# Kernel optimization log

Measured on AMD Instinct MI355X. Metric: run time of the kernel, lower is better.

Reference implementation:

```python
import jax, jax.numpy as jnp
import numpy as np

N_NODES = 100000
N_EDGES = 20000
N_PAIRS = 640000
IN_CH = 128
HEADS = 4
OUT_CH = 32


def setup_inputs() -> dict:
    key = jax.random.key(0)
    k1, k2, k3, k4, k5 = jax.random.split(key, 5)
    X = jax.random.normal(k1, (N_NODES, IN_CH), dtype=jnp.float32)
    # nn.Linear(in, H*C, bias=False); stored as [in, H*C] so X0 = X @ W
    W = jax.random.normal(k2, (IN_CH, HEADS * OUT_CH), dtype=jnp.float32) * (1.0 / np.sqrt(IN_CH))
    stdv = (6.0 / (HEADS + OUT_CH)) ** 0.5
    att_e = jax.random.uniform(k3, (1, HEADS, OUT_CH), dtype=jnp.float32, minval=-stdv, maxval=stdv)
    vertex = jax.random.randint(k4, (N_PAIRS,), 0, N_NODES, dtype=jnp.int64)
    edges = jax.random.randint(k5, (N_PAIRS,), 0, N_EDGES, dtype=jnp.int64)
    return {"X": X, "W": W, "att_e": att_e, "vertex": vertex, "edges": edges}


def reference(X, W, att_e, vertex, edges):
    N = X.shape[0]
    H, C = HEADS, OUT_CH
    X0 = X @ W                                  # [N, H*C]
    Xv_hc = X0.reshape(N, H, C)
    Xve = Xv_hc[vertex]                          # [M, H, C] gather
    # scatter-mean over hyperedges
    esum = jax.ops.segment_sum(Xve, edges, num_segments=N_EDGES)
    ecnt = jax.ops.segment_sum(jnp.ones((Xve.shape[0],), X.dtype), edges, num_segments=N_EDGES)
    Xe = esum / jnp.maximum(ecnt, 1.0)[:, None, None]   # [E, H, C]
    alpha_e = (Xe * att_e).sum(-1)               # [E, H]
    a_ev = alpha_e[edges]                        # [M, H]
    alpha = jax.nn.leaky_relu(a_ev, 0.01)
    # per-vertex softmax over incident hyperedges
    amax = jax.ops.segment_max(alpha, vertex, num_segments=N)
    alpha = jnp.exp(alpha - amax[vertex])
    asum = jax.ops.segment_sum(alpha, vertex, num_segments=N)
    alpha = alpha / (asum[vertex] + 1e-8)
    Xev = Xe[edges] * alpha[:, :, None]          # [M, H, C]
    Xv = jax.ops.segment_sum(Xev, vertex, num_segments=N)
    return Xv.reshape(N, H * C) + X0
```

## Files before the change

### kernel.cpp

```cpp
#include <hip/hip_runtime.h>
#include <hip/hip_bf16.h>

#define N_NODES 100000
#define N_EDGES 20000
#define N_PAIRS 640000
#define CH 128
#define HEADS 4
#define MAXDV 32

#define NG_GEMM 1563
#define NCHUNK 125
#define ECHUNK 5120
#define EW 5120
#define VWR 5000
#define NRANGE 5
#define VBIN_R 20000

#define OFF_X0H   0UL
#define OFF_XEH   25600000UL
#define OFF_LRE   30720000UL
#define OFF_LRV5  31360000UL
#define OFF_BLKE  34560000UL
#define OFF_BLKV  37120000UL
#define OFF_WT    50222400UL
#define OFF_ALPHA 50255168UL
#define OFF_OFFE  50575168UL
#define OFF_ENDE  50657088UL
#define OFF_OFFV  50739008UL
#define OFF_ENDV  51139008UL
#define OFF_PIDXE 51539008UL
#define OFF_PIDXV 54099008UL
#define OFF_TOT   56659008UL

typedef __attribute__((ext_vector_type(8))) short bf16x8;
typedef __attribute__((ext_vector_type(4))) float f32x4;

__device__ inline short f2bf(float f) {
    __hip_bfloat16 h = __float2bfloat16(f);
    return reinterpret_cast<short&>(h);
}
__device__ inline float bflo(unsigned w) { return __uint_as_float(w << 16); }
__device__ inline float bfhi(unsigned w) { return __uint_as_float(w & 0xffff0000u); }

__global__ __launch_bounds__(256) void k_wprep(const float* __restrict__ W,
                                               short* __restrict__ Wt,
                                               int* __restrict__ totals) {
    if (blockIdx.x == 0 && threadIdx.x < 2) totals[threadIdx.x] = 0;
    const int idx = blockIdx.x * 256 + threadIdx.x;
    const int n = idx >> 7, k = idx & 127;
    Wt[n * CH + k] = f2bf(W[k * CH + n]);
}

__device__ inline void gemm_body(int gb, const float* __restrict__ X,
                                 const short* __restrict__ Wt,
                                 short* __restrict__ X0h) {
    const int t = threadIdx.x;
    const int wave = t >> 6, lane = t & 63;
    const int r0 = gb * 64 + (wave >> 1) * 32;
    const int c0 = (wave & 1) * 64;
    const int lrow = lane & 15, lk8 = (lane >> 4) * 8;
    const int row0 = min(r0 + lrow, N_NODES - 1);
    const int row1 = min(r0 + 16 + lrow, N_NODES - 1);
    const float* px0 = &X[(size_t)row0 * CH + lk8];
    const float* px1 = &X[(size_t)row1 * CH + lk8];
    const short* pw0 = &Wt[(size_t)(c0 + lrow) * CH + lk8];

    f32x4 acc[2][4] = {};

    float4 xa[2][2]; bf16x8 bb[4];
    xa[0][0] = *(const float4*)(px0); xa[0][1] = *(const float4*)(px0 + 4);
    xa[1][0] = *(const float4*)(px1); xa[1][1] = *(const float4*)(px1 + 4);
#pragma unroll
    for (int n = 0; n < 4; ++n) bb[n] = *(const bf16x8*)(pw0 + n * 16 * CH);

#pragma unroll
    for (int kk = 0; kk < 4; ++kk) {
        float4 xn[2][2]; bf16x8 bn[4];
        if (kk < 3) {
            const int ks = (kk + 1) * 32;
            xn[0][0] = *(const float4*)(px0 + ks); xn[0][1] = *(const float4*)(px0 + ks + 4);
            xn[1][0] = *(const float4*)(px1 + ks); xn[1][1] = *(const float4*)(px1 + ks + 4);
#pragma unroll
            for (int n = 0; n < 4; ++n) bn[n] = *(const bf16x8*)(pw0 + n * 16 * CH + ks);
        }
        bf16x8 a[2];
#pragma unroll
        for (int m = 0; m < 2; ++m) {
            a[m][0] = f2bf(xa[m][0].x); a[m][1] = f2bf(xa[m][0].y);
            a[m][2] = f2bf(xa[m][0].z); a[m][3] = f2bf(xa[m][0].w);
            a[m][4] = f2bf(xa[m][1].x); a[m][5] = f2bf(xa[m][1].y);
            a[m][6] = f2bf(xa[m][1].z); a[m][7] = f2bf(xa[m][1].w);
        }
#pragma unroll
        for (int m = 0; m < 2; ++m)
#pragma unroll
            for (int n = 0; n < 4; ++n)
                acc[m][n] = __builtin_amdgcn_mfma_f32_16x16x32_bf16(a[m], bb[n], acc[m][n], 0, 0, 0);
        if (kk < 3) {
#pragma unroll
            for (int m = 0; m < 2; ++m) { xa[m][0] = xn[m][0]; xa[m][1] = xn[m][1]; }
#pragma unroll
            for (int n = 0; n < 4; ++n) bb[n] = bn[n];
        }
    }

#pragma unroll
    for (int m = 0; m < 2; ++m) {
#pragma unroll
        for (int reg = 0; reg < 4; ++reg) {
            const int row = r0 + m * 16 + (lane >> 4) * 4 + reg;
            if (row < N_NODES) {
#pragma unroll
                for (int n = 0; n < 4; ++n)
                    X0h[(size_t)row * CH + c0 + n * 16 + (lane & 15)] = f2bf(acc[m][n][reg]);
            }
        }
    }
}

__global__ __launch_bounds__(256) void k_phase1(const float* __restrict__ X,
                                                const short* __restrict__ Wt,
                                                short* __restrict__ X0h,
                                                const int* __restrict__ vertex,
                                                const int* __restrict__ edges,
                                                unsigned char* __restrict__ lrank_e,
                                                unsigned char* __restrict__ lrank_v5,
                                                unsigned int* __restrict__ blkcnt_e,
                                                unsigned int* __restrict__ blkcnt_v) {
    __shared__ unsigned int hist[EW];
    const int bid = blockIdx.x;
    const int t = threadIdx.x;

    if (bid < NRANGE * NCHUNK) {
        const int r = bid % NRANGE, c = bid / NRANGE;
        for (int i = t; i < VWR; i += 256) hist[i] = 0;
        __syncthreads();
        const int base = c * ECHUNK;
        const int vmin = r * VBIN_R;
        unsigned char* __restrict__ lr = lrank_v5 + (size_t)r * N_PAIRS;
#pragma unroll
        for (int it = 0; it < 20; ++it) {
            const int m = base + it * 256 + t;
            const int loc = vertex[m] - vmin;
            if ((unsigned)loc < (unsigned)VBIN_R) {
                const unsigned sh = (unsigned)(loc & 3) * 8u;
                unsigned old = atomicAdd(&hist[loc >> 2], 1u << sh);
                lr[m] = (unsigned char)((old >> sh) & 0xffu);
            }
        }
        __syncthreads();
        unsigned int* dst = &blkcnt_v[(size_t)(r * NCHUNK + c) * VWR];
        for (int w = t; w < VWR; w += 256) dst[w] = hist[w];
        return;
    }
    if (bid < NRANGE * NCHUNK + NCHUNK) {
        const int c = bid - NRANGE * NCHUNK;
        for (int i = t; i < EW; i += 256) hist[i] = 0;
        __syncthreads();
        const int base = c * ECHUNK;
#pragma unroll
        for (int it = 0; it < 20; ++it) {
            const int m = base + it * 256 + t;
            const int e = edges[m];
            const unsigned sh = (unsigned)(e & 3) * 8u;
            unsigned old = atomicAdd(&hist[e >> 2], 1u << sh);
            lrank_e[m] = (unsigned char)((old >> sh) & 0xffu);
        }
        __syncthreads();
        unsigned int* dst = &blkcnt_e[(size_t)c * EW];
        for (int w = t; w < EW; w += 256) dst[w] = hist[w];
        return;
    }
    gemm_body(bid - (NRANGE * NCHUNK + NCHUNK), X, Wt, X0h);
}

__global__ __launch_bounds__(256) void k_scan(unsigned int* __restrict__ blkcnt_e,
                                              unsigned int* __restrict__ blkcnt_v,
                                              int* __restrict__ off_e,
                                              int* __restrict__ end_e,
                                              int* __restrict__ off_v,
                                              int* __restrict__ end_v,
                                              int* __restrict__ totals) {
    __shared__ int s[256];
    __shared__ int base;
    const int bid = blockIdx.x, t = threadIdx.x;

    unsigned run = 0;
    int binbase = -1;
    int* off; int* end; int* total;

    if (bid < 20) {
        const int w = bid * 256 + t;
        unsigned int* p = blkcnt_e + w;
#pragma unroll 5
        for (int c = 0; c < NCHUNK; ++c) {
            const unsigned cc = *p;
            *p = run;
            run += cc;
            p += EW;
        }
        binbase = 4 * w;
        off = off_e; end = end_e; total = &totals[0];
    } else {
        off = off_v; end = end_v; total = &totals[1];
        const int id = (bid - 20) * 256 + t;
        if (id < NRANGE * VWR) {
            const int r = id / VWR, w = id % VWR;
            unsigned int* p = blkcnt_v + (size_t)r * NCHUNK * VWR + w;
#pragma unroll 5
            for (int c = 0; c < NCHUNK; ++c) {
                const unsigned cc = *p;
                *p = run;
                run += cc;
                p += VWR;
            }
            binbase = r * VBIN_R + 4 * w;
        }
    }

    const int t0 = run & 255, t1 = (run >> 8) & 255,
              t2 = (run >> 16) & 255, t3 = run >> 24;
    const int mysum = t0 + t1 + t2 + t3;
    s[t] = mysum;
    __syncthreads();
    for (int d = 1; d < 256; d <<= 1) {
        int x = (t >= d) ? s[t - d] : 0;
        __syncthreads();
        s[t] += x;
        __syncthreads();
    }
    if (t == 0) base = atomicAdd(total, s[255]);
    __syncthreads();
    if (binbase >= 0) {
        int b = base + s[t] - mysum;
        off[binbase]     = b;           end[binbase]     = b + t0;  b += t0;
        off[binbase + 1] = b;           end[binbase + 1] = b + t1;  b += t1;
        off[binbase + 2] = b;           end[binbase + 2] = b + t2;  b += t2;
        off[binbase + 3] = b;           end[binbase + 3] = b + t3;
    }
}

__global__ __launch_bounds__(256) void k_scatter(const int* __restrict__ vertex,
                                                 const int* __restrict__ edges,
                                                 const unsigned char* __restrict__ lrank_e,
                                                 const unsigned char* __restrict__ lrank_v5,
                                                 const unsigned int* __restrict__ blkcnt_e,
                                                 const unsigned int* __restrict__ blkcnt_v,
                                                 const int* __restrict__ off_e,
                                                 const int* __restrict__ off_v,
                                                 int* __restrict__ vlist_e,
                                                 int* __restrict__ elist_v) {
    const int m = blockIdx.x * 256 + threadIdx.x;
    const int e = edges[m];
    const int v = vertex[m];
    const int c = m / ECHUNK;
    const unsigned pe = blkcnt_e[(size_t)c * EW + (e >> 2)];
    const int er = (int)((pe >> ((unsigned)(e & 3) * 8u)) & 0xffu) + (int)lrank_e[m];
    const int r = v / VBIN_R, loc = v - r * VBIN_R;
    const unsigned pv = blkcnt_v[(size_t)(r * NCHUNK + c) * VWR + (loc >> 2)];
    const int vr = (int)((pv >> ((unsigned)(loc & 3) * 8u)) & 0xffu)
                 + (int)lrank_v5[(size_t)r * N_PAIRS + m];
    vlist_e[off_e[e] + er] = v;
    elist_v[off_v[v] + vr] = e;
}

__global__ __launch_bounds__(256) void k_edge(const short* __restrict__ X0h,
                                              const int* __restrict__ off_e,
                                              const int* __restrict__ end_e,
                                              const int* __restrict__ vlist,
                                              const float* __restrict__ att,
                                              short* __restrict__ Xeh,
                                              float* __restrict__ alpha_le) {
    const int t = threadIdx.x;
    const int slot = t >> 5, lane = t & 31;
    const int grp = lane >> 4, cl = lane & 15;
    const int e = blockIdx.x * 16 + slot * 2 + grp;
    const int s = off_e[e], en = end_e[e];
    const int deg = en - s;
    const short* __restrict__ xb = X0h + cl * 8;

    float va[8] = {0.f, 0.f, 0.f, 0.f, 0.f, 0.f, 0.f, 0.f};
    for (int c0 = 0; c0 < deg; c0 += 16) {
        const int cn = min(16, deg - c0);
        int vl = (cl < cn) ? (vlist[s + c0 + cl] << 7) : 0;
#pragma unroll 4
        for (int j = 0; j < cn; ++j) {
            const int vo = __shfl(vl, grp * 16 + j, 32);
            uint4 xq = *(const uint4*)(xb + vo);
            va[0] += bflo(xq.x); va[1] += bfhi(xq.x);
            va[2] += bflo(xq.y); va[3] += bfhi(xq.y);
            va[4] += bflo(xq.z); va[5] += bfhi(xq.z);
            va[6] += bflo(xq.w); va[7] += bfhi(xq.w);
        }
    }

    const float invd = 1.0f / fmaxf((float)deg, 1.0f);
    bf16x8 xh;
    float xe[8];
#pragma unroll
    for (int i = 0; i < 8; ++i) { xe[i] = va[i] * invd; xh[i] = f2bf(xe[i]); }
    *(bf16x8*)&Xeh[(size_t)e * CH + cl * 8] = xh;

    const float4 a0 = *(const float4*)&att[cl * 8];
    const float4 a1 = *(const float4*)&att[cl * 8 + 4];
    float p = xe[0] * a0.x + xe[1] * a0.y + xe[2] * a0.z + xe[3] * a0.w
            + xe[4] * a1.x + xe[5] * a1.y + xe[6] * a1.z + xe[7] * a1.w;
    p += __shfl_xor(p, 1);
    p += __shfl_xor(p, 2);
    if ((cl & 3) == 0) {
        alpha_le[e * HEADS + (cl >> 2)] = (p > 0.f) ? p : 0.01f * p;
    }
}

__global__ __launch_bounds__(256) void k_vertex(const short* __restrict__ X0h,
                                                const short* __restrict__ Xeh,
                                                const float* __restrict__ alpha_le,
                                                const int* __restrict__ off_v,
                                                const int* __restrict__ end_v,
                                                const int* __restrict__ elist,
                                                float* __restrict__ out) {
    const int t = threadIdx.x;
    const int slot = t >> 5, lane = t & 31;
    const int grp = lane >> 4, cl = lane & 15, h = cl >> 2;
    const int v = blockIdx.x * 16 + slot * 2 + grp;
    const int s = off_v[v], en = end_v[v];
    const int deg = en - s;

    __shared__ int   se[8][2][MAXDV];
    __shared__ float sa[8][2][MAXDV * HEADS];

    const short* __restrict__ xb = Xeh + cl * 8;

    float va[8] = {0.f, 0.f, 0.f, 0.f, 0.f, 0.f, 0.f, 0.f};
    if (deg <= MAXDV) {
        for (int j = cl; j < deg; j += 16) {
            const int e = elist[s + j];
            se[slot][grp][j] = e << 7;
            *(float4*)&sa[slot][grp][j << 2] = *(const float4*)&alpha_le[e * HEADS];
        }
        float mx = -INFINITY;
        for (int j = 0; j < deg; ++j) mx = fmaxf(mx, sa[slot][grp][(j << 2) + h]);
        float ssum = 0.f;
        for (int j = 0; j < deg; ++j) {
            const float p = __expf(sa[slot][grp][(j << 2) + h] - mx);
            sa[slot][grp][(j << 2) + h] = p;
            ssum += p;
        }
        const float inv = 1.0f / (ssum + 1e-8f);
        for (int j = 0; j < deg; ++j) {
            const float w = sa[slot][grp][(j << 2) + h] * inv;
            uint4 xq = *(const uint4*)(xb + se[slot][grp][j]);
            va[0] += w * bflo(xq.x); va[1] += w * bfhi(xq.x);
            va[2] += w * bflo(xq.y); va[3] += w * bfhi(xq.y);
            va[4] += w * bflo(xq.z); va[5] += w * bfhi(xq.z);
            va[6] += w * bflo(xq.w); va[7] += w * bfhi(xq.w);
        }
    } else {
        float mx = -INFINITY;
        for (int j = 0; j < deg; ++j) mx = fmaxf(mx, alpha_le[elist[s + j] * HEADS + h]);
        float ssum = 0.f;
        for (int j = 0; j < deg; ++j) ssum += __expf(alpha_le[elist[s + j] * HEADS + h] - mx);
        const float inv = 1.0f / (ssum + 1e-8f);
        for (int j = 0; j < deg; ++j) {
            const int e = elist[s + j];
            const float w = __expf(alpha_le[e * HEADS + h] - mx) * inv;
            uint4 xq = *(const uint4*)(xb + (e << 7));
            va[0] += w * bflo(xq.x); va[1] += w * bfhi(xq.x);
            va[2] += w * bflo(xq.y); va[3] += w * bfhi(xq.y);
            va[4] += w * bflo(xq.z); va[5] += w * bfhi(xq.z);
            va[6] += w * bflo(xq.w); va[7] += w * bfhi(xq.w);
        }
    }

    const uint4 rq = *(const uint4*)&X0h[(size_t)v * CH + cl * 8];
    float4 o0, o1;
    o0.x = va[0] + bflo(rq.x); o0.y = va[1] + bfhi(rq.x);
    o0.z = va[2] + bflo(rq.y); o0.w = va[3] + bfhi(rq.y);
    o1.x = va[4] + bflo(rq.z); o1.y = va[5] + bfhi(rq.z);
    o1.z = va[6] + bflo(rq.w); o1.w = va[7] + bfhi(rq.w);
    *(float4*)&out[(size_t)v * CH + cl * 8]     = o0;
    *(float4*)&out[(size_t)v * CH + cl * 8 + 4] = o1;
}

extern "C" void kernel_launch(void* const* d_in, const int* in_sizes, int n_in,
                              void* d_out, int out_size, void* d_ws, size_t ws_size,
                              hipStream_t stream) {
    const float* X      = (const float*)d_in[0];
    const float* W      = (const float*)d_in[1];
    const float* att    = (const float*)d_in[2];
    const int*   vertex = (const int*)d_in[3];
    const int*   edges  = (const int*)d_in[4];
    float* out = (float*)d_out;

    char* ws = (char*)d_ws;
    short* X0h      = (short*)(ws + OFF_X0H);
    short* Xeh      = (short*)(ws + OFF_XEH);
    unsigned char* lrank_e  = (unsigned char*)(ws + OFF_LRE);
    unsigned char* lrank_v5 = (unsigned char*)(ws + OFF_LRV5);
    unsigned int*  blkcnt_e = (unsigned int*)(ws + OFF_BLKE);
    unsigned int*  blkcnt_v = (unsigned int*)(ws + OFF_BLKV);
    short* Wt       = (short*)(ws + OFF_WT);
    float* alpha_le = (float*)(ws + OFF_ALPHA);
    int* off_e   = (int*)(ws + OFF_OFFE);
    int* end_e   = (int*)(ws + OFF_ENDE);
    int* off_v   = (int*)(ws + OFF_OFFV);
    int* end_v   = (int*)(ws + OFF_ENDV);
    int* vlist_e = (int*)(ws + OFF_PIDXE);
    int* elist_v = (int*)(ws + OFF_PIDXV);
    int* totals  = (int*)(ws + OFF_TOT);

    k_wprep<<<64, 256, 0, stream>>>(W, Wt, totals);
    k_phase1<<<NRANGE * NCHUNK + NCHUNK + NG_GEMM, 256, 0, stream>>>(
        X, Wt, X0h, vertex, edges, lrank_e, lrank_v5, blkcnt_e, blkcnt_v);
    k_scan<<<20 + 98, 256, 0, stream>>>(blkcnt_e, blkcnt_v, off_e, end_e,
                                        off_v, end_v, totals);
    k_scatter<<<N_PAIRS / 256, 256, 0, stream>>>(vertex, edges, lrank_e, lrank_v5,
                                                 blkcnt_e, blkcnt_v, off_e, off_v,
                                                 vlist_e, elist_v);
    k_edge<<<N_EDGES / 16, 256, 0, stream>>>(X0h, off_e, end_e, vlist_e, att, Xeh, alpha_le);
    k_vertex<<<N_NODES / 16, 256, 0, stream>>>(X0h, Xeh, alpha_le, off_v, end_v, elist_v, out);
}
```

Measured before the change: 144.5 us.

## Double GEMM rows per block, preload weights once, and schedule GEMM blocks first

```diff
diff --git a/kernel.cpp b/kernel.cpp
--- a/kernel.cpp
+++ b/kernel.cpp
@@ -8,7 +8,7 @@
 #define HEADS 4
 #define MAXDV 32
 
-#define NG_GEMM 1563
+#define NG2 782
 #define NCHUNK 125
 #define ECHUNK 5120
 #define EW 5120
@@ -51,68 +51,68 @@
     Wt[n * CH + k] = f2bf(W[k * CH + n]);
 }
 
-__device__ inline void gemm_body(int gb, const float* __restrict__ X,
-                                 const short* __restrict__ Wt,
-                                 short* __restrict__ X0h) {
+__device__ inline void gemm_body2(int gb, const float* __restrict__ X,
+                                  const short* __restrict__ Wt,
+                                  short* __restrict__ X0h) {
     const int t = threadIdx.x;
     const int wave = t >> 6, lane = t & 63;
-    const int r0 = gb * 64 + (wave >> 1) * 32;
     const int c0 = (wave & 1) * 64;
     const int lrow = lane & 15, lk8 = (lane >> 4) * 8;
-    const int row0 = min(r0 + lrow, N_NODES - 1);
-    const int row1 = min(r0 + 16 + lrow, N_NODES - 1);
-    const float* px0 = &X[(size_t)row0 * CH + lk8];
-    const float* px1 = &X[(size_t)row1 * CH + lk8];
     const short* pw0 = &Wt[(size_t)(c0 + lrow) * CH + lk8];
 
-    f32x4 acc[2][4] = {};
-
-    float4 xa[2][2]; bf16x8 bb[4];
-    xa[0][0] = *(const float4*)(px0); xa[0][1] = *(const float4*)(px0 + 4);
-    xa[1][0] = *(const float4*)(px1); xa[1][1] = *(const float4*)(px1 + 4);
-#pragma unroll
-    for (int n = 0; n < 4; ++n) bb[n] = *(const bf16x8*)(pw0 + n * 16 * CH);
-
-#pragma unroll
-    for (int kk = 0; kk < 4; ++kk) {
-        float4 xn[2][2]; bf16x8 bn[4];
-        if (kk < 3) {
-            const int ks = (kk + 1) * 32;
-            xn[0][0] = *(const float4*)(px0 + ks); xn[0][1] = *(const float4*)(px0 + ks + 4);
-            xn[1][0] = *(const float4*)(px1 + ks); xn[1][1] = *(const float4*)(px1 + ks + 4);
-#pragma unroll
-            for (int n = 0; n < 4; ++n) bn[n] = *(const bf16x8*)(pw0 + n * 16 * CH + ks);
-        }
-        bf16x8 a[2];
+    bf16x8 B[4][4];
+#pragma unroll
+    for (int kk = 0; kk < 4; ++kk)
+#pragma unroll
+        for (int n = 0; n < 4; ++n)
+            B[kk][n] = *(const bf16x8*)(pw0 + n * 16 * CH + kk * 32);
+
+#pragma unroll
+    for (int half = 0; half < 2; ++half) {
+        const int r0 = gb * 128 + half * 64 + (wave >> 1) * 32;
+        const int row0 = min(r0 + lrow, N_NODES - 1);
+        const int row1 = min(r0 + 16 + lrow, N_NODES - 1);
+        const float* px0 = &X[(size_t)row0 * CH + lk8];
+        const float* px1 = &X[(size_t)row1 * CH + lk8];
+
+        float4 xa0[4][2], xa1[4][2];
+#pragma unroll
+        for (int kk = 0; kk < 4; ++kk) {
+            xa0[kk][0] = *(const float4*)(px0 + kk * 32);
+            xa0[kk][1] = *(const float4*)(px0 + kk * 32 + 4);
+            xa1[kk][0] = *(const float4*)(px1 + kk * 32);
+            xa1[kk][1] = *(const float4*)(px1 + kk * 32 + 4);
+        }
+
+        f32x4 acc[2][4] = {};
+#pragma unroll
+        for (int kk = 0; kk < 4; ++kk) {
+            bf16x8 a[2];
+            a[0][0] = f2bf(xa0[kk][0].x); a[0][1] = f2bf(xa0[kk][0].y);
+            a[0][2] = f2bf(xa0[kk][0].z); a[0][3] = f2bf(xa0[kk][0].w);
+            a[0][4] = f2bf(xa0[kk][1].x); a[0][5] = f2bf(xa0[kk][1].y);
+            a[0][6] = f2bf(xa0[kk][1].z); a[0][7] = f2bf(xa0[kk][1].w);
+            a[1][0] = f2bf(xa1[kk][0].x); a[1][1] = f2bf(xa1[kk][0].y);
+            a[1][2] = f2bf(xa1[kk][0].z); a[1][3] = f2bf(xa1[kk][0].w);
+            a[1][4] = f2bf(xa1[kk][1].x); a[1][5] = f2bf(xa1[kk][1].y);
+            a[1][6] = f2bf(xa1[kk][1].z); a[1][7] = f2bf(xa1[kk][1].w);
+#pragma unroll
+            for (int m = 0; m < 2; ++m)
+#pragma unroll
+                for (int n = 0; n < 4; ++n)
+                    acc[m][n] = __builtin_amdgcn_mfma_f32_16x16x32_bf16(a[m], B[kk][n], acc[m][n], 0, 0, 0);
+        }
+
 #pragma unroll
         for (int m = 0; m < 2; ++m) {
-            a[m][0] = f2bf(xa[m][0].x); a[m][1] = f2bf(xa[m][0].y);
-            a[m][2] = f2bf(xa[m][0].z); a[m][3] = f2bf(xa[m][0].w);
-            a[m][4] = f2bf(xa[m][1].x); a[m][5] = f2bf(xa[m][1].y);
-            a[m][6] = f2bf(xa[m][1].z); a[m][7] = f2bf(xa[m][1].w);
-        }
-#pragma unroll
-        for (int m = 0; m < 2; ++m)
-#pragma unroll
-            for (int n = 0; n < 4; ++n)
-                acc[m][n] = __builtin_amdgcn_mfma_f32_16x16x32_bf16(a[m], bb[n], acc[m][n], 0, 0, 0);
-        if (kk < 3) {
-#pragma unroll
-            for (int m = 0; m < 2; ++m) { xa[m][0] = xn[m][0]; xa[m][1] = xn[m][1]; }
-#pragma unroll
-            for (int n = 0; n < 4; ++n) bb[n] = bn[n];
-        }
-    }
-
-#pragma unroll
-    for (int m = 0; m < 2; ++m) {
-#pragma unroll
-        for (int reg = 0; reg < 4; ++reg) {
-            const int row = r0 + m * 16 + (lane >> 4) * 4 + reg;
-            if (row < N_NODES) {
-#pragma unroll
-                for (int n = 0; n < 4; ++n)
-                    X0h[(size_t)row * CH + c0 + n * 16 + (lane & 15)] = f2bf(acc[m][n][reg]);
+#pragma unroll
+            for (int reg = 0; reg < 4; ++reg) {
+                const int row = r0 + m * 16 + (lane >> 4) * 4 + reg;
+                if (row < N_NODES) {
+#pragma unroll
+                    for (int n = 0; n < 4; ++n)
+                        X0h[(size_t)row * CH + c0 + n * 16 + (lane & 15)] = f2bf(acc[m][n][reg]);
+                }
             }
         }
     }
@@ -131,8 +131,13 @@
     const int bid = blockIdx.x;
     const int t = threadIdx.x;
 
-    if (bid < NRANGE * NCHUNK) {
-        const int r = bid % NRANGE, c = bid / NRANGE;
+    if (bid < NG2) {
+        gemm_body2(bid, X, Wt, X0h);
+        return;
+    }
+    const int r2 = bid - NG2;
+    if (r2 < NRANGE * NCHUNK) {
+        const int r = r2 % NRANGE, c = r2 / NRANGE;
         for (int i = t; i < VWR; i += 256) hist[i] = 0;
         __syncthreads();
         const int base = c * ECHUNK;
@@ -153,25 +158,21 @@
         for (int w = t; w < VWR; w += 256) dst[w] = hist[w];
         return;
     }
-    if (bid < NRANGE * NCHUNK + NCHUNK) {
-        const int c = bid - NRANGE * NCHUNK;
-        for (int i = t; i < EW; i += 256) hist[i] = 0;
-        __syncthreads();
-        const int base = c * ECHUNK;
-#pragma unroll
-        for (int it = 0; it < 20; ++it) {
-            const int m = base + it * 256 + t;
-            const int e = edges[m];
-            const unsigned sh = (unsigned)(e & 3) * 8u;
-            unsigned old = atomicAdd(&hist[e >> 2], 1u << sh);
-            lrank_e[m] = (unsigned char)((old >> sh) & 0xffu);
-        }
-        __syncthreads();
-        unsigned int* dst = &blkcnt_e[(size_t)c * EW];
-        for (int w = t; w < EW; w += 256) dst[w] = hist[w];
-        return;
-    }
-    gemm_body(bid - (NRANGE * NCHUNK + NCHUNK), X, Wt, X0h);
+    const int c = r2 - NRANGE * NCHUNK;
+    for (int i = t; i < EW; i += 256) hist[i] = 0;
+    __syncthreads();
+    const int base = c * ECHUNK;
+#pragma unroll
+    for (int it = 0; it < 20; ++it) {
+        const int m = base + it * 256 + t;
+        const int e = edges[m];
+        const unsigned sh = (unsigned)(e & 3) * 8u;
+        unsigned old = atomicAdd(&hist[e >> 2], 1u << sh);
+        lrank_e[m] = (unsigned char)((old >> sh) & 0xffu);
+    }
+    __syncthreads();
+    unsigned int* dst = &blkcnt_e[(size_t)c * EW];
+    for (int w = t; w < EW; w += 256) dst[w] = hist[w];
 }
 
 __global__ __launch_bounds__(256) void k_scan(unsigned int* __restrict__ blkcnt_e,
@@ -410,7 +411,7 @@
     int* totals  = (int*)(ws + OFF_TOT);
 
     k_wprep<<<64, 256, 0, stream>>>(W, Wt, totals);
-    k_phase1<<<NRANGE * NCHUNK + NCHUNK + NG_GEMM, 256, 0, stream>>>(
+    k_phase1<<<NG2 + NRANGE * NCHUNK + NCHUNK, 256, 0, stream>>>(
         X, Wt, X0h, vertex, edges, lrank_e, lrank_v5, blkcnt_e, blkcnt_v);
     k_scan<<<20 + 98, 256, 0, stream>>>(blkcnt_e, blkcnt_v, off_e, end_e,
                                         off_v, end_v, totals);
```

Measured after the change: 142.1 us. No clear change (-1.6%).
